# Optimization experiments

Hardware: AMD Instinct MI355X
Metric: run time of the kernel (lower is better)

The kernel has to match this reference:

```python
import jax, jax.numpy as jnp
import numpy as np

ALPHA = 0.6
K = 4


def gsdnef_conv(x, edge_index, W, b, alpha, K):
    """SpGSDNEFConv: linear transform then K-step graph-signal-denoising diffusion
    h_{k+1} = (x + alpha * A_hat h_k) / (1 + alpha), A_hat = D^-1/2 (A+I) D^-1/2."""
    n = x.shape[0]
    x = x @ W + b  # [N, C_out]
    loop = jnp.arange(n, dtype=edge_index.dtype)
    src = jnp.concatenate([edge_index[0], loop])
    dst = jnp.concatenate([edge_index[1], loop])
    ones = jnp.ones(src.shape, dtype=x.dtype)
    deg = jax.ops.segment_sum(ones, dst, num_segments=n)
    dinv = jax.lax.rsqrt(jnp.maximum(deg, 1e-12))
    norm = dinv[src] * dinv[dst]  # [E+N]
    inv = 1.0 / (1.0 + alpha)
    h = x
    for _ in range(K):
        agg = jax.ops.segment_sum(h[src] * norm[:, None], dst, num_segments=n)
        h = (x + alpha * agg) * inv
    return h


def setup_inputs() -> dict:
    key = jax.random.key(0)
    ks = jax.random.split(key, 16)
    N, E, C_in, H, C_out = 50000, 800000, 256, 128, 64
    x = jax.random.normal(ks[0], (N, C_in), dtype=jnp.float32)
    edge_index = jax.random.randint(ks[1], (2, E), 0, N, dtype=jnp.int64)

    def lin(k, fan_in, fan_out):
        k1, k2 = jax.random.split(k)
        bound = 1.0 / np.sqrt(fan_in)
        W = jax.random.uniform(k1, (fan_in, fan_out), jnp.float32, -bound, bound)
        b = jax.random.uniform(k2, (fan_out,), jnp.float32, -bound, bound)
        return W, b

    Wc1, bc1 = lin(ks[2], C_in, H)
    Wl1, bl1 = lin(ks[3], C_in, H)
    Wc2, bc2 = lin(ks[4], H, H)
    Wl2, bl2 = lin(ks[5], H, H)
    Wc3, bc3 = lin(ks[6], H, C_out)
    Wl3, bl3 = lin(ks[7], H, C_out)
    return dict(x=x, edge_index=edge_index,
                Wc1=Wc1, bc1=bc1, Wl1=Wl1, bl1=bl1,
                Wc2=Wc2, bc2=bc2, Wl2=Wl2, bl2=bl2,
                Wc3=Wc3, bc3=bc3, Wl3=Wl3, bl3=bl3)


def reference(x, edge_index, Wc1, bc1, Wl1, bl1, Wc2, bc2, Wl2, bl2, Wc3, bc3, Wl3, bl3):
    h = jax.nn.elu(gsdnef_conv(x, edge_index, Wc1, bc1, ALPHA, K) + (x @ Wl1 + bl1))
    h = jax.nn.elu(gsdnef_conv(h, edge_index, Wc2, bc2, ALPHA, K) + (h @ Wl2 + bl2))
    h = gsdnef_conv(h, edge_index, Wc3, bc3, ALPHA, K) + (h @ Wl3 + bl3)
    return h
```

## Files before the change

kernel.cpp:

```cpp
#include <hip/hip_runtime.h>
#include <hip/hip_fp16.h>
#include <math.h>

#define ALPHA_C 0.6f

typedef _Float16 f16;
typedef f16 f16x8 __attribute__((ext_vector_type(8)));
typedef float f32x4 __attribute__((ext_vector_type(4)));

__global__ void detect_idx_kernel(const void* __restrict__ ei, int* __restrict__ flag,
                                  int E, int N) {
    int i = blockIdx.x * blockDim.x + threadIdx.x;
    if (i >= E) return;
    long long v = ((const long long*)ei)[i];
    if (v < 0 || v >= (long long)N) *flag = 1;
}

__global__ void convert_count_kernel(const void* __restrict__ ei, const int* __restrict__ flag,
                                     int* __restrict__ out, int* __restrict__ cnt,
                                     int E, int n2e) {
    int i = blockIdx.x * blockDim.x + threadIdx.x;
    if (i >= n2e) return;
    int v;
    if (*flag == 0)
        v = (int)((const long long*)ei)[i];
    else
        v = ((const int*)ei)[i];
    out[i] = v;
    if (i >= E) atomicAdd(&cnt[v], 1);
}

__global__ void dinv_kernel(const int* __restrict__ cnt, float* __restrict__ dinv, int N) {
    int i = blockIdx.x * blockDim.x + threadIdx.x;
    if (i < N) dinv[i] = rsqrtf((float)cnt[i] + 1.0f);
}

__global__ void block_reduce_kernel(const int* __restrict__ cnt, int* __restrict__ bsum, int n) {
    __shared__ int s[256];
    int tid = threadIdx.x;
    int i = blockIdx.x * 256 + tid;
    int v = (i < n) ? cnt[i] : 0;
    s[tid] = v;
    __syncthreads();
    for (int o = 128; o > 0; o >>= 1) {
        if (tid < o) s[tid] += s[tid + o];
        __syncthreads();
    }
    if (tid == 0) bsum[blockIdx.x] = s[0];
}

__global__ void scan_top_kernel(int* __restrict__ bsum, int nb) {
    __shared__ int s[1024];
    int tid = threadIdx.x;
    int v = (tid < nb) ? bsum[tid] : 0;
    s[tid] = v;
    __syncthreads();
    for (int o = 1; o < 1024; o <<= 1) {
        int t = (tid >= o) ? s[tid - o] : 0;
        __syncthreads();
        s[tid] += t;
        __syncthreads();
    }
    if (tid < nb) bsum[tid] = s[tid] - v;
}

__global__ void scan_fill_kernel(const int* __restrict__ cnt, const int* __restrict__ bsum,
                                 int* __restrict__ row_off, int n) {
    __shared__ int s[256];
    int tid = threadIdx.x;
    int i = blockIdx.x * 256 + tid;
    int v = (i < n) ? cnt[i] : 0;
    s[tid] = v;
    __syncthreads();
    for (int o = 1; o < 256; o <<= 1) {
        int t = (tid >= o) ? s[tid - o] : 0;
        __syncthreads();
        s[tid] += t;
        __syncthreads();
    }
    int base = bsum[blockIdx.x];
    if (i < n) row_off[i] = base + s[tid] - v;
    if (i == n - 1) row_off[n] = base + s[tid];
}

__global__ void fill_kernel(const int* __restrict__ src, const int* __restrict__ dst,
                            const float* __restrict__ dinv, const int* __restrict__ row_off,
                            int* __restrict__ cursor, unsigned int* __restrict__ csre, int E) {
    int e = blockIdx.x * blockDim.x + threadIdx.x;
    if (e >= E) return;
    int d = dst[e], s = src[e];
    int pos = atomicAdd(&cursor[d], 1);
    int idx = row_off[d] + pos;
    float w = dinv[s] * dinv[d];
    csre[idx] = (unsigned int)s |
                ((unsigned int)__half_as_ushort(__float2half(w)) << 16);
}

__global__ void prep_all_w_kernel(
    const float* __restrict__ Wc1, const float* __restrict__ Wl1,
    const float* __restrict__ Wc2, const float* __restrict__ Wl2,
    const float* __restrict__ Wc3, const float* __restrict__ Wl3,
    f16* __restrict__ w1c, f16* __restrict__ w1l,
    f16* __restrict__ w2c, f16* __restrict__ w2l,
    f16* __restrict__ w3c, f16* __restrict__ w3l) {
    int i = blockIdx.x * blockDim.x + threadIdx.x;
    const float* W; f16* O; int K, Nn, base;
    if      (i <  32768) { W = Wc1; O = w1c; K = 256; Nn = 128; base = i; }
    else if (i <  65536) { W = Wl1; O = w1l; K = 256; Nn = 128; base = i - 32768; }
    else if (i <  81920) { W = Wc2; O = w2c; K = 128; Nn = 128; base = i - 65536; }
    else if (i <  98304) { W = Wl2; O = w2l; K = 128; Nn = 128; base = i - 81920; }
    else if (i < 106496) { W = Wc3; O = w3c; K = 128; Nn = 64;  base = i - 98304; }
    else if (i < 114688) { W = Wl3; O = w3l; K = 128; Nn = 64;  base = i - 106496; }
    else return;
    int k = base / Nn, n = base - k * Nn;
    O[(size_t)n * K + k] = (f16)W[base];
}

template <int K, int NH, int AMODE>
__global__ __launch_bounds__(256) void gemm2_kernel(
    const void* __restrict__ A0v, const void* __restrict__ A1v,
    const f16* __restrict__ WtA, const f16* __restrict__ WtB,
    const float* __restrict__ biasA, const float* __restrict__ biasB,
    f16* __restrict__ CA, f16* __restrict__ CB, int M) {
    constexpr int NT = 2 * NH / 16;
    int tid = threadIdx.x;
    int wave = tid >> 6, lane = tid & 63;
    int lr = lane & 15, lhi = lane >> 4;
    int m0 = blockIdx.x * 64;

    int arow = m0 + wave * 16 + lr;
    int arow_c = arow < M ? arow : (M - 1);

    f32x4 acc[NT];
#pragma unroll
    for (int n = 0; n < NT; ++n) acc[n] = (f32x4){0.f, 0.f, 0.f, 0.f};

    size_t aoff = (size_t)arow_c * K + lhi * 8;
    size_t woff = (size_t)lr * K + lhi * 8;

#pragma unroll 2
    for (int ks = 0; ks < K; ks += 32) {
        f16x8 a;
        if constexpr (AMODE == 0) {
            a = *(const f16x8*)((const f16*)A0v + aoff + ks);
        } else if constexpr (AMODE == 1) {
            const float* xp = (const float*)A0v + aoff + ks;
            float4 a0 = *(const float4*)xp;
            float4 a1 = *(const float4*)(xp + 4);
            a[0] = (f16)a0.x; a[1] = (f16)a0.y; a[2] = (f16)a0.z; a[3] = (f16)a0.w;
            a[4] = (f16)a1.x; a[5] = (f16)a1.y; a[6] = (f16)a1.z; a[7] = (f16)a1.w;
        } else {
            f16x8 u0 = *(const f16x8*)((const f16*)A0v + aoff + ks);
            f16x8 u1 = *(const f16x8*)((const f16*)A1v + aoff + ks);
#pragma unroll
            for (int j = 0; j < 8; ++j) {
                float t = (float)u0[j] + (float)u1[j];
                a[j] = (f16)(t > 0.f ? t : expm1f(t));
            }
        }
#pragma unroll
        for (int n = 0; n < NT; ++n) {
            const f16* wp = (n < NT / 2)
                ? (WtA + (size_t)n * 16 * K)
                : (WtB + (size_t)(n - NT / 2) * 16 * K);
            f16x8 b = *(const f16x8*)(wp + woff + ks);
            acc[n] = __builtin_amdgcn_mfma_f32_16x16x32_f16(a, b, acc[n], 0, 0, 0);
        }
    }

    int rbase = m0 + wave * 16 + lhi * 4;
#pragma unroll
    for (int n = 0; n < NT; ++n) {
        bool isA = (n < NT / 2);
        int colg = (isA ? n : n - NT / 2) * 16 + lr;
        f16* outp = isA ? CA : CB;
        float bv = (isA ? biasA : biasB)[colg];
#pragma unroll
        for (int r = 0; r < 4; ++r) {
            int row = rbase + r;
            if (row < M) outp[(size_t)row * NH + colg] = (f16)(acc[n][r] + bv);
        }
    }
}

template <int C, bool FINAL>
__global__ __launch_bounds__(256) void diffuse16_kernel(
    const __half* __restrict__ h, const __half* __restrict__ xc,
    const float* __restrict__ dinv, const int* __restrict__ row_off,
    const unsigned int* __restrict__ csre, __half* __restrict__ hout,
    const f16* __restrict__ lin, float* __restrict__ fout, int N) {
    const float inv = 1.0f / (1.0f + ALPHA_C);
    int gid = blockIdx.x * blockDim.x + threadIdx.x;
    int node = gid >> 6;
    if (node >= N) return;
    int lane = threadIdx.x & 63;
    float di = dinv[node];
    float di2 = di * di;
    int e0 = row_off[node], e1 = row_off[node + 1];

    if constexpr (C == 128) {
        int l = lane & 15, grp = lane >> 4;
        float acc[8];
#pragma unroll
        for (int i = 0; i < 8; ++i) acc[i] = 0.f;
        size_t coff = (size_t)l * 8;

        if (grp == 0) {
            float4 rv = *(const float4*)(h + ((size_t)node << 7) + coff);
            const __half2* p = (const __half2*)&rv;
#pragma unroll
            for (int k = 0; k < 4; ++k) {
                float2 f = __half22float2(p[k]);
                acc[2 * k] += di2 * f.x;
                acc[2 * k + 1] += di2 * f.y;
            }
        }
        int e = e0 + grp;
        for (; e + 12 < e1; e += 16) {
            unsigned int ev0 = csre[e], ev1 = csre[e + 4], ev2 = csre[e + 8], ev3 = csre[e + 12];
            float4 r0 = *(const float4*)(h + ((size_t)(ev0 & 0xFFFF) << 7) + coff);
            float4 r1 = *(const float4*)(h + ((size_t)(ev1 & 0xFFFF) << 7) + coff);
            float4 r2 = *(const float4*)(h + ((size_t)(ev2 & 0xFFFF) << 7) + coff);
            float4 r3 = *(const float4*)(h + ((size_t)(ev3 & 0xFFFF) << 7) + coff);
            float w0 = __half2float(__ushort_as_half((unsigned short)(ev0 >> 16)));
            float w1 = __half2float(__ushort_as_half((unsigned short)(ev1 >> 16)));
            float w2 = __half2float(__ushort_as_half((unsigned short)(ev2 >> 16)));
            float w3 = __half2float(__ushort_as_half((unsigned short)(ev3 >> 16)));
            const __half2* p0 = (const __half2*)&r0;
            const __half2* p1 = (const __half2*)&r1;
            const __half2* p2 = (const __half2*)&r2;
            const __half2* p3 = (const __half2*)&r3;
#pragma unroll
            for (int k = 0; k < 4; ++k) {
                float2 f0 = __half22float2(p0[k]);
                float2 f1 = __half22float2(p1[k]);
                float2 f2 = __half22float2(p2[k]);
                float2 f3 = __half22float2(p3[k]);
                acc[2 * k]     += w0 * f0.x + w1 * f1.x + w2 * f2.x + w3 * f3.x;
                acc[2 * k + 1] += w0 * f0.y + w1 * f1.y + w2 * f2.y + w3 * f3.y;
            }
        }
        for (; e < e1; e += 4) {
            unsigned int ev0 = csre[e];
            float4 r0 = *(const float4*)(h + ((size_t)(ev0 & 0xFFFF) << 7) + coff);
            float w0 = __half2float(__ushort_as_half((unsigned short)(ev0 >> 16)));
            const __half2* p0 = (const __half2*)&r0;
#pragma unroll
            for (int k = 0; k < 4; ++k) {
                float2 f0 = __half22float2(p0[k]);
                acc[2 * k]     += w0 * f0.x;
                acc[2 * k + 1] += w0 * f0.y;
            }
        }
#pragma unroll
        for (int i = 0; i < 8; ++i) {
            acc[i] += __shfl_xor(acc[i], 16);
            acc[i] += __shfl_xor(acc[i], 32);
        }
        if (grp == 0) {
            float4 xv = *(const float4*)(xc + ((size_t)node << 7) + coff);
            const __half2* xp = (const __half2*)&xv;
            __half ov[8];
#pragma unroll
            for (int k = 0; k < 4; ++k) {
                float2 xf = __half22float2(xp[k]);
                ov[2 * k]     = __float2half((xf.x + ALPHA_C * acc[2 * k]) * inv);
                ov[2 * k + 1] = __float2half((xf.y + ALPHA_C * acc[2 * k + 1]) * inv);
            }
            *(float4*)(hout + ((size_t)node << 7) + coff) = *(float4*)ov;
        }
    } else {
        int l = lane & 7, grp = lane >> 3;
        float acc[8];
#pragma unroll
        for (int i = 0; i < 8; ++i) acc[i] = 0.f;
        size_t coff = (size_t)l * 8;

        if (grp == 0) {
            float4 rv = *(const float4*)(h + ((size_t)node << 6) + coff);
            const __half2* p = (const __half2*)&rv;
#pragma unroll
            for (int k = 0; k < 4; ++k) {
                float2 f = __half22float2(p[k]);
                acc[2 * k] += di2 * f.x;
                acc[2 * k + 1] += di2 * f.y;
            }
        }
        int e = e0 + grp;
        for (; e + 8 < e1; e += 16) {
            unsigned int ev0 = csre[e], ev1 = csre[e + 8];
            float4 r0 = *(const float4*)(h + ((size_t)(ev0 & 0xFFFF) << 6) + coff);
            float4 r1 = *(const float4*)(h + ((size_t)(ev1 & 0xFFFF) << 6) + coff);
            float w0 = __half2float(__ushort_as_half((unsigned short)(ev0 >> 16)));
            float w1 = __half2float(__ushort_as_half((unsigned short)(ev1 >> 16)));
            const __half2* p0 = (const __half2*)&r0;
            const __half2* p1 = (const __half2*)&r1;
#pragma unroll
            for (int k = 0; k < 4; ++k) {
                float2 f0 = __half22float2(p0[k]);
                float2 f1 = __half22float2(p1[k]);
                acc[2 * k]     += w0 * f0.x + w1 * f1.x;
                acc[2 * k + 1] += w0 * f0.y + w1 * f1.y;
            }
        }
        if (e < e1) {
            unsigned int ev0 = csre[e];
            float4 r0 = *(const float4*)(h + ((size_t)(ev0 & 0xFFFF) << 6) + coff);
            float w0 = __half2float(__ushort_as_half((unsigned short)(ev0 >> 16)));
            const __half2* p0 = (const __half2*)&r0;
#pragma unroll
            for (int k = 0; k < 4; ++k) {
                float2 f0 = __half22float2(p0[k]);
                acc[2 * k]     += w0 * f0.x;
                acc[2 * k + 1] += w0 * f0.y;
            }
        }
#pragma unroll
        for (int i = 0; i < 8; ++i) {
            acc[i] += __shfl_xor(acc[i], 8);
            acc[i] += __shfl_xor(acc[i], 16);
            acc[i] += __shfl_xor(acc[i], 32);
        }
        if (grp == 0) {
            float4 xv = *(const float4*)(xc + ((size_t)node << 6) + coff);
            const __half2* xp = (const __half2*)&xv;
            float r[8];
#pragma unroll
            for (int k = 0; k < 4; ++k) {
                float2 xf = __half22float2(xp[k]);
                r[2 * k]     = (xf.x + ALPHA_C * acc[2 * k]) * inv;
                r[2 * k + 1] = (xf.y + ALPHA_C * acc[2 * k + 1]) * inv;
            }
            if constexpr (FINAL) {
                f16x8 lv = *(const f16x8*)(lin + ((size_t)node << 6) + coff);
                float4 o0, o1;
                o0.x = r[0] + (float)lv[0]; o0.y = r[1] + (float)lv[1];
                o0.z = r[2] + (float)lv[2]; o0.w = r[3] + (float)lv[3];
                o1.x = r[4] + (float)lv[4]; o1.y = r[5] + (float)lv[5];
                o1.z = r[6] + (float)lv[6]; o1.w = r[7] + (float)lv[7];
                float* op = fout + ((size_t)node << 6) + coff;
                *(float4*)op = o0;
                *(float4*)(op + 4) = o1;
            } else {
                __half ov[8];
#pragma unroll
                for (int k = 0; k < 8; ++k) ov[k] = __float2half(r[k]);
                *(float4*)(hout + ((size_t)node << 6) + coff) = *(float4*)ov;
            }
        }
    }
}

extern "C" void kernel_launch(void* const* d_in, const int* in_sizes, int n_in,
                              void* d_out, int out_size, void* d_ws, size_t ws_size,
                              hipStream_t stream) {
    const float* x   = (const float*)d_in[0];
    const void*  ei  = d_in[1];
    const float* Wc1 = (const float*)d_in[2];  const float* bc1 = (const float*)d_in[3];
    const float* Wl1 = (const float*)d_in[4];  const float* bl1 = (const float*)d_in[5];
    const float* Wc2 = (const float*)d_in[6];  const float* bc2 = (const float*)d_in[7];
    const float* Wl2 = (const float*)d_in[8];  const float* bl2 = (const float*)d_in[9];
    const float* Wc3 = (const float*)d_in[10]; const float* bc3 = (const float*)d_in[11];
    const float* Wl3 = (const float*)d_in[12]; const float* bl3 = (const float*)d_in[13];
    float* out = (float*)d_out;

    const int N = in_sizes[0] / 256;
    const int E = in_sizes[1] / 2;

    size_t off = 0;
    auto alloc = [&](size_t bytes) {
        void* p = (char*)d_ws + off;
        off += (bytes + 255) & ~(size_t)255;
        return p;
    };
    f16* B0 = (f16*)alloc((size_t)N * 128 * 2);
    f16* B1 = (f16*)alloc((size_t)N * 128 * 2);
    f16* B2 = (f16*)alloc((size_t)N * 128 * 2);
    f16* B3 = (f16*)alloc((size_t)N * 128 * 2);
    f16* B4 = (f16*)alloc((size_t)N * 128 * 2);
    f16* wt1c = (f16*)alloc((size_t)256 * 128 * 2);
    f16* wt1l = (f16*)alloc((size_t)256 * 128 * 2);
    f16* wt2c = (f16*)alloc((size_t)128 * 128 * 2);
    f16* wt2l = (f16*)alloc((size_t)128 * 128 * 2);
    f16* wt3c = (f16*)alloc((size_t)128 * 64 * 2);
    f16* wt3l = (f16*)alloc((size_t)128 * 64 * 2);
    float* dinv   = (float*)alloc((size_t)N * 4);
    int*   cnt    = (int*)  alloc((size_t)N * 4);
    int*   rowoff = (int*)  alloc((size_t)(N + 1) * 4);
    int*   bsum   = (int*)  alloc(1024 * 4);
    unsigned int* csre = (unsigned int*)alloc((size_t)E * 4);
    int*   idx32  = (int*)  alloc((size_t)2 * E * 4);
    int*   flag   = (int*)  alloc(4);
    int* src32 = idx32;
    int* dst32 = idx32 + E;

    const int TB = 256;
    int ge  = (E + TB - 1) / TB;
    int g2e = (2 * E + TB - 1) / TB;
    int gn  = (N + TB - 1) / TB;
    int nb  = (N + 255) / 256;

    hipMemsetAsync(flag, 0, 4, stream);
    hipMemsetAsync(cnt, 0, (size_t)N * 4, stream);
    detect_idx_kernel<<<ge, TB, 0, stream>>>(ei, flag, E, N);
    convert_count_kernel<<<g2e, TB, 0, stream>>>(ei, flag, idx32, cnt, E, 2 * E);

    dinv_kernel<<<gn, TB, 0, stream>>>(cnt, dinv, N);
    block_reduce_kernel<<<nb, 256, 0, stream>>>(cnt, bsum, N);
    scan_top_kernel<<<1, 1024, 0, stream>>>(bsum, nb);
    scan_fill_kernel<<<nb, 256, 0, stream>>>(cnt, bsum, rowoff, N);
    hipMemsetAsync(cnt, 0, (size_t)N * 4, stream);
    fill_kernel<<<ge, TB, 0, stream>>>(src32, dst32, dinv, rowoff, cnt, csre, E);

    prep_all_w_kernel<<<(114688 + TB - 1) / TB, TB, 0, stream>>>(
        Wc1, Wl1, Wc2, Wl2, Wc3, Wl3, wt1c, wt1l, wt2c, wt2l, wt3c, wt3l);

    int gm = (N + 63) / 64;
    int gd = (N * 64 + TB - 1) / TB;

    gemm2_kernel<256, 128, 1><<<gm, TB, 0, stream>>>(x, nullptr, wt1c, wt1l, bc1, bl1, B0, B1, N);
    diffuse16_kernel<128, false><<<gd, TB, 0, stream>>>((__half*)B0, (__half*)B0, dinv, rowoff, csre, (__half*)B2, nullptr, nullptr, N);
    diffuse16_kernel<128, false><<<gd, TB, 0, stream>>>((__half*)B2, (__half*)B0, dinv, rowoff, csre, (__half*)B3, nullptr, nullptr, N);
    diffuse16_kernel<128, false><<<gd, TB, 0, stream>>>((__half*)B3, (__half*)B0, dinv, rowoff, csre, (__half*)B2, nullptr, nullptr, N);
    diffuse16_kernel<128, false><<<gd, TB, 0, stream>>>((__half*)B2, (__half*)B0, dinv, rowoff, csre, (__half*)B3, nullptr, nullptr, N);

    gemm2_kernel<128, 128, 2><<<gm, TB, 0, stream>>>(B3, B1, wt2c, wt2l, bc2, bl2, B0, B4, N);
    diffuse16_kernel<128, false><<<gd, TB, 0, stream>>>((__half*)B0, (__half*)B0, dinv, rowoff, csre, (__half*)B1, nullptr, nullptr, N);
    diffuse16_kernel<128, false><<<gd, TB, 0, stream>>>((__half*)B1, (__half*)B0, dinv, rowoff, csre, (__half*)B2, nullptr, nullptr, N);
    diffuse16_kernel<128, false><<<gd, TB, 0, stream>>>((__half*)B2, (__half*)B0, dinv, rowoff, csre, (__half*)B1, nullptr, nullptr, N);
    diffuse16_kernel<128, false><<<gd, TB, 0, stream>>>((__half*)B1, (__half*)B0, dinv, rowoff, csre, (__half*)B2, nullptr, nullptr, N);

    gemm2_kernel<128, 64, 2><<<gm, TB, 0, stream>>>(B2, B4, wt3c, wt3l, bc3, bl3, B0, B1, N);
    diffuse16_kernel<64, false><<<gd, TB, 0, stream>>>((__half*)B0, (__half*)B0, dinv, rowoff, csre, (__half*)B2, nullptr, nullptr, N);
    diffuse16_kernel<64, false><<<gd, TB, 0, stream>>>((__half*)B2, (__half*)B0, dinv, rowoff, csre, (__half*)B3, nullptr, nullptr, N);
    diffuse16_kernel<64, false><<<gd, TB, 0, stream>>>((__half*)B3, (__half*)B0, dinv, rowoff, csre, (__half*)B2, nullptr, nullptr, N);
    diffuse16_kernel<64, true ><<<gd, TB, 0, stream>>>((__half*)B2, (__half*)B0, dinv, rowoff, csre, nullptr, B1, out, N);
}
```

Baseline: 626.8 us.

## Stage weight tiles in LDS and compute two row tiles per wave in GEMM

The dual-output GEMM now cooperatively loads 64-wide K slices of both weight matrices into shared memory once per block. Each wave computes two 16-row tiles that reuse every B fragment, so the block covers 128 rows and the grid is halved. This cuts redundant global or L2 weight reads per row tile, at the cost of more accumulator registers, sync barriers and up to 32KB of LDS, which may lower occupancy. The GEMMs are a small part of a pipeline that is mostly diffusion passes.

Result: faster. 578.2 us (-7.8%).

```diff
diff --git a/kernel.cpp b/kernel.cpp
--- a/kernel.cpp
+++ b/kernel.cpp
@@ -123,62 +123,96 @@
     const float* __restrict__ biasA, const float* __restrict__ biasB,
     f16* __restrict__ CA, f16* __restrict__ CB, int M) {
     constexpr int NT = 2 * NH / 16;
+    constexpr int BM = 128;
+    __shared__ f16 Wlds[NT * 1024];
+
     int tid = threadIdx.x;
-    int wave = tid >> 6, lane = tid & 63;
+    int wv = tid >> 6, lane = tid & 63;
     int lr = lane & 15, lhi = lane >> 4;
-    int m0 = blockIdx.x * 64;
-
-    int arow = m0 + wave * 16 + lr;
-    int arow_c = arow < M ? arow : (M - 1);
-
-    f32x4 acc[NT];
-#pragma unroll
-    for (int n = 0; n < NT; ++n) acc[n] = (f32x4){0.f, 0.f, 0.f, 0.f};
-
-    size_t aoff = (size_t)arow_c * K + lhi * 8;
-    size_t woff = (size_t)lr * K + lhi * 8;
-
-#pragma unroll 2
-    for (int ks = 0; ks < K; ks += 32) {
-        f16x8 a;
-        if constexpr (AMODE == 0) {
-            a = *(const f16x8*)((const f16*)A0v + aoff + ks);
-        } else if constexpr (AMODE == 1) {
-            const float* xp = (const float*)A0v + aoff + ks;
-            float4 a0 = *(const float4*)xp;
-            float4 a1 = *(const float4*)(xp + 4);
-            a[0] = (f16)a0.x; a[1] = (f16)a0.y; a[2] = (f16)a0.z; a[3] = (f16)a0.w;
-            a[4] = (f16)a1.x; a[5] = (f16)a1.y; a[6] = (f16)a1.z; a[7] = (f16)a1.w;
-        } else {
-            f16x8 u0 = *(const f16x8*)((const f16*)A0v + aoff + ks);
-            f16x8 u1 = *(const f16x8*)((const f16*)A1v + aoff + ks);
-#pragma unroll
-            for (int j = 0; j < 8; ++j) {
-                float t = (float)u0[j] + (float)u1[j];
-                a[j] = (f16)(t > 0.f ? t : expm1f(t));
-            }
-        }
-#pragma unroll
-        for (int n = 0; n < NT; ++n) {
-            const f16* wp = (n < NT / 2)
-                ? (WtA + (size_t)n * 16 * K)
-                : (WtB + (size_t)(n - NT / 2) * 16 * K);
-            f16x8 b = *(const f16x8*)(wp + woff + ks);
-            acc[n] = __builtin_amdgcn_mfma_f32_16x16x32_f16(a, b, acc[n], 0, 0, 0);
-        }
-    }
-
-    int rbase = m0 + wave * 16 + lhi * 4;
-#pragma unroll
-    for (int n = 0; n < NT; ++n) {
-        bool isA = (n < NT / 2);
-        int colg = (isA ? n : n - NT / 2) * 16 + lr;
-        f16* outp = isA ? CA : CB;
-        float bv = (isA ? biasA : biasB)[colg];
-#pragma unroll
-        for (int r = 0; r < 4; ++r) {
-            int row = rbase + r;
-            if (row < M) outp[(size_t)row * NH + colg] = (f16)(acc[n][r] + bv);
+    int m0 = blockIdx.x * BM;
+
+    f32x4 acc[2][NT];
+#pragma unroll
+    for (int s = 0; s < 2; ++s)
+#pragma unroll
+        for (int t = 0; t < NT; ++t) acc[s][t] = (f32x4){0.f, 0.f, 0.f, 0.f};
+
+    int ar0 = m0 + wv * 32 + lr;
+    int ar1 = ar0 + 16;
+    ar0 = ar0 < M ? ar0 : M - 1;
+    ar1 = ar1 < M ? ar1 : M - 1;
+    size_t aoff0 = (size_t)ar0 * K + lhi * 8;
+    size_t aoff1 = (size_t)ar1 * K + lhi * 8;
+
+    for (int k0 = 0; k0 < K; k0 += 64) {
+        for (int c = tid; c < NT * 128; c += 256) {
+            int t = c >> 7;
+            int rem = c & 127;
+            int ks = rem >> 6, kh = (rem >> 4) & 3, r = rem & 15;
+            int nloc = (t < NT / 2) ? t : t - NT / 2;
+            const f16* srcp = ((t < NT / 2) ? WtA : WtB)
+                              + (size_t)(nloc * 16 + r) * K + k0 + ks * 32 + kh * 8;
+            *(f16x8*)&Wlds[(size_t)c * 8] = *(const f16x8*)srcp;
+        }
+        __syncthreads();
+
+        f16x8 a[2][2];
+#pragma unroll
+        for (int s = 0; s < 2; ++s) {
+            size_t ao = s ? aoff1 : aoff0;
+#pragma unroll
+            for (int ks = 0; ks < 2; ++ks) {
+                size_t idx = ao + k0 + ks * 32;
+                if constexpr (AMODE == 0) {
+                    a[s][ks] = *(const f16x8*)((const f16*)A0v + idx);
+                } else if constexpr (AMODE == 1) {
+                    const float* xp = (const float*)A0v + idx;
+                    float4 a0 = *(const float4*)xp;
+                    float4 a1 = *(const float4*)(xp + 4);
+                    f16x8 v;
+                    v[0] = (f16)a0.x; v[1] = (f16)a0.y; v[2] = (f16)a0.z; v[3] = (f16)a0.w;
+                    v[4] = (f16)a1.x; v[5] = (f16)a1.y; v[6] = (f16)a1.z; v[7] = (f16)a1.w;
+                    a[s][ks] = v;
+                } else {
+                    f16x8 u0 = *(const f16x8*)((const f16*)A0v + idx);
+                    f16x8 u1 = *(const f16x8*)((const f16*)A1v + idx);
+                    f16x8 v;
+#pragma unroll
+                    for (int j = 0; j < 8; ++j) {
+                        float tt = (float)u0[j] + (float)u1[j];
+                        v[j] = (f16)(tt > 0.f ? tt : expm1f(tt));
+                    }
+                    a[s][ks] = v;
+                }
+            }
+        }
+
+#pragma unroll
+        for (int ks = 0; ks < 2; ++ks) {
+#pragma unroll
+            for (int t = 0; t < NT; ++t) {
+                f16x8 b = *(const f16x8*)&Wlds[(size_t)(t * 128 + ks * 64 + lane) * 8];
+                acc[0][t] = __builtin_amdgcn_mfma_f32_16x16x32_f16(a[0][ks], b, acc[0][t], 0, 0, 0);
+                acc[1][t] = __builtin_amdgcn_mfma_f32_16x16x32_f16(a[1][ks], b, acc[1][t], 0, 0, 0);
+            }
+        }
+        __syncthreads();
+    }
+
+#pragma unroll
+    for (int s = 0; s < 2; ++s) {
+        int rbase = m0 + wv * 32 + s * 16 + lhi * 4;
+#pragma unroll
+        for (int t = 0; t < NT; ++t) {
+            bool isA = (t < NT / 2);
+            int colg = (isA ? t : t - NT / 2) * 16 + lr;
+            f16* outp = isA ? CA : CB;
+            float bv = (isA ? biasA : biasB)[colg];
+#pragma unroll
+            for (int r = 0; r < 4; ++r) {
+                int row = rbase + r;
+                if (row < M) outp[(size_t)row * NH + colg] = (f16)(acc[s][t][r] + bv);
+            }
         }
     }
 }
@@ -415,7 +449,7 @@
     prep_all_w_kernel<<<(114688 + TB - 1) / TB, TB, 0, stream>>>(
         Wc1, Wl1, Wc2, Wl2, Wc3, Wl3, wt1c, wt1l, wt2c, wt2l, wt3c, wt3l);
 
-    int gm = (N + 63) / 64;
+    int gm = (N + 127) / 128;
     int gd = (N * 64 + TB - 1) / TB;
 
     gemm2_kernel<256, 128, 1><<<gm, TB, 0, stream>>>(x, nullptr, wt1c, wt1l, bc1, bl1, B0, B1, N);
```
